# Optimization experiments

Measured on AMD Instinct MI355X. Metric: run time of the kernel, lower is better.

The kernel has to match this reference:

```python
import jax, jax.numpy as jnp
import numpy as np

B, D = 131072, 256            # batch, n_features
ND, NA = 64, 64               # decision_dim, attention_dim
UN = ND + NA                  # GLU units (feature transformer width)
NSTEPS = 3
RELAX = 1.3                   # relaxation_factor
BN_EPS = 1e-3                 # keras BatchNormalization default epsilon
OUT_DIM = 64
SQRT_HALF = float(np.sqrt(0.5))

def _bn(x, g, b, m, v):
    # inference-mode batch norm with moving statistics
    return (x - m) * jax.lax.rsqrt(v + BN_EPS) * g + b

def _glu(x, W, g, b, m, v):
    h = _bn(x @ W, g, b, m, v)            # [B, 2*UN]
    return h[:, :UN] * jax.nn.sigmoid(h[:, UN:])

def _sparsemax(z):
    zs = -jnp.sort(-z, axis=-1)           # descending sort
    k = jnp.arange(1, z.shape[-1] + 1, dtype=z.dtype)
    zc = jnp.cumsum(zs, axis=-1)
    kz = jnp.sum((1.0 + k * zs > zc).astype(jnp.int32), axis=-1, keepdims=True)
    tau = (jnp.take_along_axis(zc, kz - 1, axis=-1) - 1.0) / kz.astype(z.dtype)
    return jnp.maximum(z - tau, 0.0)

def _shared_block(x, W0, W1, g, b, m, v):
    # input dim D != UN -> omit first residual
    h = _glu(x, W0, g[0], b[0], m[0], v[0])
    h2 = _glu(h, W1, g[1], b[1], m[1], v[1])
    return SQRT_HALF * (h + h2)

def _dep_block(x, W, g, b, m, v):
    # input dim UN == UN -> residual on every layer
    for i in range(2):
        h = _glu(x, W[i], g[i], b[i], m[i], v[i])
        x = SQRT_HALF * (x + h)
    return x

def setup_inputs() -> dict:
    key = jax.random.key(0)
    ks = jax.random.split(key, 16)
    s_in = 1.0 / np.sqrt(D)
    s_un = 1.0 / np.sqrt(UN)
    s_na = 1.0 / np.sqrt(NA)
    def bn_params(k, shape):
        k1, k2 = jax.random.split(k)
        return (jax.random.uniform(k1, shape, jnp.float32, 0.5, 1.5),
                0.1 * jax.random.normal(k2, shape, jnp.float32),
                jnp.zeros(shape, jnp.float32), jnp.ones(shape, jnp.float32))
    in_g, in_b, in_m, in_v = bn_params(ks[0], (D,))
    sh_W0 = s_in * jax.random.normal(ks[1], (D, 2 * UN), jnp.float32)
    sh_W1 = s_un * jax.random.normal(ks[2], (UN, 2 * UN), jnp.float32)
    sh_g, sh_b, sh_m, sh_v = bn_params(ks[3], (2, 2 * UN))
    dep_W = s_un * jax.random.normal(ks[4], (NSTEPS + 1, 2, UN, 2 * UN), jnp.float32)
    dep_g, dep_b, dep_m, dep_v = bn_params(ks[5], (NSTEPS + 1, 2, 2 * UN))
    at_W = s_na * jax.random.normal(ks[6], (NSTEPS, NA, D), jnp.float32)
    at_g, at_b, at_m, at_v = bn_params(ks[7], (NSTEPS, D))
    Wout = (1.0 / np.sqrt(ND)) * jax.random.normal(ks[8], (ND, OUT_DIM), jnp.float32)
    inputs = jax.random.normal(ks[9], (B, D), jnp.float32)
    return dict(inputs=inputs, in_g=in_g, in_b=in_b, in_m=in_m, in_v=in_v,
                sh_W0=sh_W0, sh_W1=sh_W1, sh_g=sh_g, sh_b=sh_b, sh_m=sh_m, sh_v=sh_v,
                dep_W=dep_W, dep_g=dep_g, dep_b=dep_b, dep_m=dep_m, dep_v=dep_v,
                at_W=at_W, at_g=at_g, at_b=at_b, at_m=at_m, at_v=at_v, Wout=Wout)

def reference(inputs, in_g, in_b, in_m, in_v, sh_W0, sh_W1, sh_g, sh_b, sh_m, sh_v,
              dep_W, dep_g, dep_b, dep_m, dep_v, at_W, at_g, at_b, at_m, at_v, Wout):
    features = _bn(inputs, in_g, in_b, in_m, in_v)          # initial BN, [B, D]
    # initial feature transformer (step 0 split, only attention part used)
    x = _shared_block(features, sh_W0, sh_W1, sh_g, sh_b, sh_m, sh_v)
    x = _dep_block(x, dep_W[0], dep_g[0], dep_b[0], dep_m[0], dep_v[0])
    a = x[:, ND:]                                           # [B, NA]
    prior = jnp.ones_like(features)
    out_agg = jnp.zeros((inputs.shape[0], ND), inputs.dtype)
    for s in range(NSTEPS):
        logits = _bn(a @ at_W[s], at_g[s], at_b[s], at_m[s], at_v[s])  # [B, D]
        mask = _sparsemax(prior * logits)
        prior = prior * (RELAX - mask)
        x = _shared_block(mask * features, sh_W0, sh_W1, sh_g, sh_b, sh_m, sh_v)
        x = _dep_block(x, dep_W[s + 1], dep_g[s + 1], dep_b[s + 1], dep_m[s + 1], dep_v[s + 1])
        out_agg = out_agg + jax.nn.relu(x[:, :ND])
        a = x[:, ND:]
    return out_agg @ Wout                                   # [B, OUT_DIM]
```

## Files before the change

kernel.cpp:

```cpp
#include <hip/hip_runtime.h>
#include <hip/hip_bf16.h>
#include <hip/hip_fp16.h>

typedef unsigned short u16;
typedef __attribute__((ext_vector_type(8))) short short8;
typedef __attribute__((ext_vector_type(4))) float f32x4;

#define BN_EPS    1e-3f
#define RELAX     1.3f
#define SQRT_HALF 0.7071067811865476f

#define PK_G0_US     0
#define PK_G1_US     65536
#define PK_DEP_US    98304
#define PK_AT_US     360448
#define PK_WOUT_US   409600
#define PK_WOUTLO_US 413696
#define OFF_SHIFT 835584
#define OFF_SCALE 848896
#define OFF_INSC  862208
#define OFF_INSH  863232

__device__ __forceinline__ u16 f2bf(float x){
  unsigned u = __float_as_uint(x);
  return (u16)((u + 0x7fffu + ((u >> 16) & 1u)) >> 16);
}
__device__ __forceinline__ float bf2f(u16 h){ return __uint_as_float(((unsigned)h) << 16); }
__device__ __forceinline__ float sigm(float x){ return 1.0f / (1.0f + __expf(-x)); }
__device__ __forceinline__ f32x4 splat4(float x){ f32x4 v; v[0]=x; v[1]=x; v[2]=x; v[3]=x; return v; }

__device__ __forceinline__ unsigned pk2(float a, float b){
  float2 t; t.x = a; t.y = b;
  union { __hip_bfloat162 h; unsigned u; } v;
  v.h = __float22bfloat162_rn(t);
  return v.u;
}
__device__ __forceinline__ f32x4 unpk4(uint2 p){
  f32x4 r;
  r[0] = __uint_as_float(p.x << 16);
  r[1] = __uint_as_float(p.x & 0xffff0000u);
  r[2] = __uint_as_float(p.y << 16);
  r[3] = __uint_as_float(p.y & 0xffff0000u);
  return r;
}
__device__ __forceinline__ float2 h2f2(unsigned u){
  union { unsigned u; __half2 h; } v; v.u = u;
  return __half22float2(v.h);
}
__device__ __forceinline__ unsigned f22h2(float a, float b){
  union { __half2 h; unsigned u; } v; v.h = __floats2half2_rn(a, b);
  return v.u;
}

__global__ void prep_bn(
  const float* in_g, const float* in_b, const float* in_m, const float* in_v,
  const float* sh_g, const float* sh_b, const float* sh_m, const float* sh_v,
  const float* dep_g, const float* dep_b, const float* dep_m, const float* dep_v,
  const float* at_g, const float* at_b, const float* at_m, const float* at_v,
  float* shiftT, float* scaleT, float* inSc, float* inSh)
{
  int r = blockIdx.x, f = threadIdx.x;
  if (r < 13) {
    const float *g, *bb, *mm, *vv;
    if (r < 2)       { g = sh_g + r*256;        bb = sh_b + r*256;        mm = sh_m + r*256;        vv = sh_v + r*256; }
    else if (r < 10) { int j = r-2;  g = dep_g + j*256; bb = dep_b + j*256; mm = dep_m + j*256; vv = dep_v + j*256; }
    else             { int j = r-10; g = at_g  + j*256; bb = at_b  + j*256; mm = at_m  + j*256; vv = at_v  + j*256; }
    float sc = g[f] * rsqrtf(vv[f] + BN_EPS);
    scaleT[r*256 + f] = sc;
    shiftT[r*256 + f] = bb[f] - mm[f]*sc;
  } else {
    float sc = in_g[f] * rsqrtf(in_v[f] + BN_EPS);
    inSc[f] = sc;
    inSh[f] = in_b[f] - in_m[f]*sc;
  }
}

__global__ void prep_pack(
  const float* sh_W0, const float* sh_W1, const float* dep_W,
  const float* at_W, const float* Wout, const float* scaleT, u16* pk)
{
  int c = blockIdx.x*256 + threadIdx.x;
  const float* W; int K, Nout, srow, base; bool lo = false;
  if (c < 8192)       { W = sh_W0; K = 256; Nout = 256; srow = 0;  base = 0; }
  else if (c < 12288) { W = sh_W1; K = 128; Nout = 256; srow = 1;  base = 8192; }
  else if (c < 45056) { int j = (c-12288) >> 12; W = dep_W + j*32768; K = 128; Nout = 256; srow = 2+j;  base = 12288 + j*4096; }
  else if (c < 51200) { int j = (c-45056) >> 11; W = at_W  + j*16384; K = 64;  Nout = 256; srow = 10+j; base = 45056 + j*2048; }
  else if (c < 51712) { W = Wout; K = 64; Nout = 64; srow = -1; base = 51200; }
  else                { W = Wout; K = 64; Nout = 64; srow = -1; base = 51712; lo = true; }
  int local = c - base;
  int lane  = local & 63;
  int t     = local >> 6;
  int KS    = K >> 5;
  int lsh   = (K == 256) ? 3 : (K == 128) ? 2 : 1;
  int ks    = t & (KS - 1);
  int mf    = t >> lsh;
  int feat  = mf*16 + (lane & 15);
  int k0    = ks*32 + ((lane >> 4) << 3);
  float scl = (srow < 0) ? 1.0f : scaleT[srow*256 + feat];
  u16 v[8];
  #pragma unroll
  for (int j = 0; j < 8; ++j) {
    float x = W[(size_t)(k0 + j)*Nout + feat] * scl;
    u16 h = f2bf(x);
    if (lo) h = f2bf(x - bf2f(h));
    v[j] = h;
  }
  ushort4* d4 = (ushort4*)(pk + (size_t)c*8);
  ushort4 p0; p0.x=v[0]; p0.y=v[1]; p0.z=v[2]; p0.w=v[3];
  ushort4 p1; p1.x=v[4]; p1.y=v[5]; p1.z=v[6]; p1.w=v[7];
  d4[0] = p0; d4[1] = p1;
}

template<int KS, int LDB, int KOFF>
__device__ __forceinline__ void gemm4(const u16* __restrict__ pk, const u16* bufB,
                                      int w, int l15, int lg, int swzv, f32x4 acc[4][2])
{
  const int lane = lg*16 + l15;
  short8 ae[4], be[2], ao[4], bo[2];
  #pragma unroll
  for (int nf = 0; nf < 2; ++nf) {
    int idx = (nf*16 + l15)*LDB + KOFF + lg*8;
    be[nf] = *(const short8*)(bufB + (idx ^ swzv));
  }
  #pragma unroll
  for (int mi = 0; mi < 4; ++mi)
    ae[mi] = *(const short8*)(pk + (size_t)(((w + 4*mi)*KS)*64 + lane)*8);

  #pragma unroll 1
  for (int ks = 0; ks < KS; ks += 2) {
    #pragma unroll
    for (int nf = 0; nf < 2; ++nf) {
      int idx = (nf*16 + l15)*LDB + KOFF + (ks+1)*32 + lg*8;
      bo[nf] = *(const short8*)(bufB + (idx ^ swzv));
    }
    #pragma unroll
    for (int mi = 0; mi < 4; ++mi)
      ao[mi] = *(const short8*)(pk + (size_t)(((w + 4*mi)*KS + ks + 1)*64 + lane)*8);
    #pragma unroll
    for (int mi = 0; mi < 4; ++mi) {
      acc[mi][0] = __builtin_amdgcn_mfma_f32_16x16x32_bf16(ae[mi], be[0], acc[mi][0], 0, 0, 0);
      acc[mi][1] = __builtin_amdgcn_mfma_f32_16x16x32_bf16(ae[mi], be[1], acc[mi][1], 0, 0, 0);
    }
    if (ks + 2 < KS) {
      #pragma unroll
      for (int nf = 0; nf < 2; ++nf) {
        int idx = (nf*16 + l15)*LDB + KOFF + (ks+2)*32 + lg*8;
        be[nf] = *(const short8*)(bufB + (idx ^ swzv));
      }
      #pragma unroll
      for (int mi = 0; mi < 4; ++mi)
        ae[mi] = *(const short8*)(pk + (size_t)(((w + 4*mi)*KS + ks + 2)*64 + lane)*8);
    }
    #pragma unroll
    for (int mi = 0; mi < 4; ++mi) {
      acc[mi][0] = __builtin_amdgcn_mfma_f32_16x16x32_bf16(ao[mi], bo[0], acc[mi][0], 0, 0, 0);
      acc[mi][1] = __builtin_amdgcn_mfma_f32_16x16x32_bf16(ao[mi], bo[1], acc[mi][1], 0, 0, 0);
    }
  }
}

__device__ __forceinline__ void zero4(f32x4 acc[4][2]){
  #pragma unroll
  for (int mi = 0; mi < 4; ++mi)
    #pragma unroll
    for (int nf = 0; nf < 2; ++nf)
      acc[mi][nf] = splat4(0.0f);
}

__device__ __forceinline__ void glu_epi4(const f32x4 acc[4][2], const float* __restrict__ shrow,
                                         int w, int lg, f32x4 h[2][2])
{
  #pragma unroll
  for (int mi = 0; mi < 2; ++mi) {
    const int f0 = (w + 4*mi)*16 + lg*4;
    const f32x4 bh = *(const f32x4*)(shrow + f0);
    const f32x4 bg = *(const f32x4*)(shrow + f0 + 128);
    #pragma unroll
    for (int nf = 0; nf < 2; ++nf)
      #pragma unroll
      for (int c = 0; c < 4; ++c) {
        float v = acc[mi][nf][c] + bh[c];
        float g = acc[mi+2][nf][c] + bg[c];
        h[mi][nf][c] = v * sigm(g);
      }
  }
}

__device__ __forceinline__ void write_half(u16* dst, const f32x4 v[2][2], int w, int l15, int lg, int swzv)
{
  #pragma unroll
  for (int mi = 0; mi < 2; ++mi) {
    const int f0 = (w + 4*mi)*16 + lg*4;
    #pragma unroll
    for (int nf = 0; nf < 2; ++nf) {
      const int s = nf*16 + l15;
      uint2 p;
      p.x = pk2(v[mi][nf][0], v[mi][nf][1]);
      p.y = pk2(v[mi][nf][2], v[mi][nf][3]);
      *(uint2*)(dst + ((s*128 + f0) ^ swzv)) = p;
    }
  }
}

__device__ __forceinline__ void shared_dep(const u16* __restrict__ pk, const float* __restrict__ shiftT,
                                           const u16* binput, u16* big, u16* hbuf, int inv,
                                           int w, int l15, int lg, int swzv)
{
  f32x4 acc[4][2];
  zero4(acc);
  gemm4<8, 256, 0>(pk + PK_G0_US, binput, w, l15, lg, swzv, acc);
  {
    f32x4 h[2][2];
    glu_epi4(acc, shiftT + 0, w, lg, h);
    write_half(hbuf, h, w, l15, lg, swzv);
  }
  __syncthreads();

  zero4(acc);
  gemm4<4, 128, 0>(pk + PK_G1_US, hbuf, w, l15, lg, swzv, acc);
  {
    f32x4 h2[2][2];
    glu_epi4(acc, shiftT + 256, w, lg, h2);
    f32x4 xv[2][2];
    #pragma unroll
    for (int mi = 0; mi < 2; ++mi) {
      const int f0 = (w + 4*mi)*16 + lg*4;
      #pragma unroll
      for (int nf = 0; nf < 2; ++nf) {
        const int s = nf*16 + l15;
        uint2 hp = *(const uint2*)(hbuf + ((s*128 + f0) ^ swzv));
        f32x4 hv = unpk4(hp);
        xv[mi][nf] = (hv + h2[mi][nf]) * SQRT_HALF;
      }
    }
    write_half(big, xv, w, l15, lg, swzv);
  }
  __syncthreads();

  const u16* xin = big;
  u16* xout = big + 4096;
  #pragma unroll
  for (int i = 0; i < 2; ++i) {
    zero4(acc);
    gemm4<4, 128, 0>(pk + PK_DEP_US + (inv*2 + i)*32768, xin, w, l15, lg, swzv, acc);
    f32x4 hd[2][2];
    glu_epi4(acc, shiftT + (2 + inv*2 + i)*256, w, lg, hd);
    #pragma unroll
    for (int mi = 0; mi < 2; ++mi) {
      const int f0 = (w + 4*mi)*16 + lg*4;
      #pragma unroll
      for (int nf = 0; nf < 2; ++nf) {
        const int s = nf*16 + l15;
        uint2 xp = *(const uint2*)(xin + ((s*128 + f0) ^ swzv));
        f32x4 xo = unpk4(xp);
        hd[mi][nf] = (xo + hd[mi][nf]) * SQRT_HALF;
      }
    }
    write_half(xout, hd, w, l15, lg, swzv);
    __syncthreads();
    const u16* t = xin; xin = xout; xout = (u16*)t;
  }
}

__global__ void __launch_bounds__(256, 2)
tabnet_main(const float* __restrict__ inp, const u16* __restrict__ pk,
            const float* __restrict__ shiftT, const float* __restrict__ inSc,
            const float* __restrict__ inSh, float* __restrict__ out)
{
  __shared__ __align__(16) u16 feat[32*256];
  __shared__ __align__(16) u16 big[32*256];
  __shared__ __align__(16) u16 hbuf[32*128];
  __shared__ unsigned priorS[16*256];
  __shared__ float    aggS[8*256];
  float2* red2 = (float2*)hbuf;

  const int tid  = threadIdx.x;
  const int w    = tid >> 6;
  const int lane = tid & 63;
  const int l15  = lane & 15, lg = lane >> 4;
  const int swzv = (l15 & 7) << 3;
  const long long row0 = (long long)blockIdx.x * 32;

  {
    const int f = lane*4;
    const f32x4 sc = *(const f32x4*)(inSc + f);
    const f32x4 sh = *(const f32x4*)(inSh + f);
    #pragma unroll
    for (int j = 0; j < 8; ++j) {
      const int s = j*4 + w;
      f32x4 v = *(const f32x4*)(inp + (row0 + s)*256 + f);
      uint2 p;
      p.x = pk2(v[0]*sc[0] + sh[0], v[1]*sc[1] + sh[1]);
      p.y = pk2(v[2]*sc[2] + sh[2], v[3]*sc[3] + sh[3]);
      *(uint2*)(feat + ((s*256 + f) ^ ((s & 7) << 3))) = p;
    }
  }
  {
    const unsigned one2 = 0x3c003c00u;
    #pragma unroll
    for (int j = 0; j < 16; ++j) priorS[j*256 + tid] = one2;
    #pragma unroll
    for (int j = 0; j < 8; ++j) aggS[j*256 + tid] = 0.0f;
  }
  __syncthreads();

  shared_dep(pk, shiftT, feat, big, hbuf, 0, w, l15, lg, swzv);

  #pragma unroll 1
  for (int st = 0; st < 3; ++st) {
    f32x4 z[4][2];
    zero4(z);
    gemm4<2, 128, 64>(pk + PK_AT_US + st*16384, big, w, l15, lg, swzv, z);
    #pragma unroll
    for (int mi = 0; mi < 4; ++mi) {
      const f32x4 bz = *(const f32x4*)(shiftT + (10 + st)*256 + (w + 4*mi)*16 + lg*4);
      #pragma unroll
      for (int nf = 0; nf < 2; ++nf) {
        float2 p0 = h2f2(priorS[((mi<<2)|(nf<<1)|0)*256 + tid]);
        float2 p1 = h2f2(priorS[((mi<<2)|(nf<<1)|1)*256 + tid]);
        z[mi][nf][0] = (z[mi][nf][0] + bz[0]) * p0.x;
        z[mi][nf][1] = (z[mi][nf][1] + bz[1]) * p0.y;
        z[mi][nf][2] = (z[mi][nf][2] + bz[2]) * p1.x;
        z[mi][nf][3] = (z[mi][nf][3] + bz[3]) * p1.y;
      }
    }

    float tau[2];
    {
      #pragma unroll
      for (int nf = 0; nf < 2; ++nf) {
        float m = -1e30f;
        #pragma unroll
        for (int mi = 0; mi < 4; ++mi)
          #pragma unroll
          for (int c = 0; c < 4; ++c) m = fmaxf(m, z[mi][nf][c]);
        m = fmaxf(m, __shfl_xor(m, 16, 64));
        m = fmaxf(m, __shfl_xor(m, 32, 64));
        if (lg == 0) { int si = nf*16 + l15; red2[si*9 + w].x = m; }
      }
      __syncthreads();
      #pragma unroll
      for (int nf = 0; nf < 2; ++nf) {
        const int si = nf*16 + l15;
        float m = fmaxf(fmaxf(red2[si*9+0].x, red2[si*9+1].x),
                        fmaxf(red2[si*9+2].x, red2[si*9+3].x));
        tau[nf] = m - 1.0f;
      }
    }

    int buf = 0;
    #pragma unroll 1
    for (int it = 0; it < 12; ++it) {
      buf ^= 1;
      float S[2], C[2];
      #pragma unroll
      for (int nf = 0; nf < 2; ++nf) {
        f32x4 s4 = splat4(0.0f), c4 = splat4(0.0f);
        #pragma unroll
        for (int mi = 0; mi < 4; ++mi)
          #pragma unroll
          for (int c = 0; c < 4; ++c) {
            float d = z[mi][nf][c] - tau[nf];
            s4[c] += fmaxf(d, 0.0f);
            c4[c] += (d > 0.0f) ? 1.0f : 0.0f;
          }
        float S_ = (s4[0] + s4[1]) + (s4[2] + s4[3]);
        float C_ = (c4[0] + c4[1]) + (c4[2] + c4[3]);
        S_ += __shfl_xor(S_, 16, 64); S_ += __shfl_xor(S_, 32, 64);
        C_ += __shfl_xor(C_, 16, 64); C_ += __shfl_xor(C_, 32, 64);
        S[nf] = S_; C[nf] = C_;
      }
      if (lg == 0) {
        #pragma unroll
        for (int nf = 0; nf < 2; ++nf) {
          int si = nf*16 + l15;
          float2 p; p.x = S[nf]; p.y = C[nf];
          red2[buf*288 + si*9 + w] = p;
        }
      }
      __syncthreads();
      bool ok = true;
      float tauN[2];
      #pragma unroll
      for (int nf = 0; nf < 2; ++nf) {
        const int si = nf*16 + l15;
        float Ss = 0.0f, Cs = 0.0f;
        #pragma unroll
        for (int i = 0; i < 4; ++i) { float2 p = red2[buf*288 + si*9 + i]; Ss += p.x; Cs += p.y; }
        ok = ok && (fabsf(Ss - 1.0f) < 1e-5f);
        tauN[nf] = tau[nf] + (Ss - 1.0f) / Cs;
      }
      if (__all(ok)) break;
      #pragma unroll
      for (int nf = 0; nf < 2; ++nf) tau[nf] = tauN[nf];
    }

    #pragma unroll
    for (int mi = 0; mi < 4; ++mi) {
      const int f0 = (w + 4*mi)*16 + lg*4;
      #pragma unroll
      for (int nf = 0; nf < 2; ++nf) {
        const int si = nf*16 + l15;
        ushort4 fv = *(const ushort4*)(feat + ((si*256 + f0) ^ swzv));
        float m0 = fmaxf(z[mi][nf][0] - tau[nf], 0.0f);
        float m1 = fmaxf(z[mi][nf][1] - tau[nf], 0.0f);
        float m2 = fmaxf(z[mi][nf][2] - tau[nf], 0.0f);
        float m3 = fmaxf(z[mi][nf][3] - tau[nf], 0.0f);
        const int j0 = ((mi<<2)|(nf<<1)|0)*256 + tid;
        const int j1 = ((mi<<2)|(nf<<1)|1)*256 + tid;
        float2 p0 = h2f2(priorS[j0]);
        float2 p1 = h2f2(priorS[j1]);
        priorS[j0] = f22h2(p0.x * (RELAX - m0), p0.y * (RELAX - m1));
        priorS[j1] = f22h2(p1.x * (RELAX - m2), p1.y * (RELAX - m3));
        uint2 p;
        p.x = pk2(bf2f(fv.x) * m0, bf2f(fv.y) * m1);
        p.y = pk2(bf2f(fv.z) * m2, bf2f(fv.w) * m3);
        *(uint2*)(big + ((si*256 + f0) ^ swzv)) = p;
      }
    }
    __syncthreads();

    shared_dep(pk, shiftT, big, big, hbuf, st + 1, w, l15, lg, swzv);

    #pragma unroll
    for (int nf = 0; nf < 2; ++nf) {
      const int si = nf*16 + l15;
      const int f0 = w*16 + lg*4;
      uint2 xp = *(const uint2*)(big + ((si*128 + f0) ^ swzv));
      f32x4 xv = unpk4(xp);
      #pragma unroll
      for (int c = 0; c < 4; ++c)
        aggS[(nf*4 + c)*256 + tid] += fmaxf(xv[c], 0.0f);
    }
  }

  __syncthreads();
  {
    #pragma unroll
    for (int nf = 0; nf < 2; ++nf) {
      const int si = nf*16 + l15;
      const int f0 = w*16 + lg*4;
      float a0 = aggS[(nf*4+0)*256 + tid];
      float a1 = aggS[(nf*4+1)*256 + tid];
      float a2 = aggS[(nf*4+2)*256 + tid];
      float a3 = aggS[(nf*4+3)*256 + tid];
      ushort4 hi, lo;
      u16 h0 = f2bf(a0); hi.x = h0; lo.x = f2bf(a0 - bf2f(h0));
      u16 h1 = f2bf(a1); hi.y = h1; lo.y = f2bf(a1 - bf2f(h1));
      u16 h2v = f2bf(a2); hi.z = h2v; lo.z = f2bf(a2 - bf2f(h2v));
      u16 h3 = f2bf(a3); hi.w = h3; lo.w = f2bf(a3 - bf2f(h3));
      *(ushort4*)(big + ((si*64 + f0) ^ swzv)) = hi;
      *(ushort4*)(big + 2048 + ((si*64 + f0) ^ swzv)) = lo;
    }
  }
  __syncthreads();

  {
    const int lane64 = lg*16 + l15;
    f32x4 facc[2];
    facc[0] = splat4(0.0f); facc[1] = splat4(0.0f);
    #pragma unroll
    for (int ks = 0; ks < 2; ++ks) {
      short8 aHi = *(const short8*)(pk + PK_WOUT_US   + (size_t)((w*2 + ks)*64 + lane64)*8);
      short8 aLo = *(const short8*)(pk + PK_WOUTLO_US + (size_t)((w*2 + ks)*64 + lane64)*8);
      #pragma unroll
      for (int j = 0; j < 2; ++j) {
        const int si = j*16 + l15;
        short8 bHi = *(const short8*)(big + ((si*64 + ks*32 + lg*8) ^ swzv));
        short8 bLo = *(const short8*)(big + 2048 + ((si*64 + ks*32 + lg*8) ^ swzv));
        facc[j] = __builtin_amdgcn_mfma_f32_16x16x32_bf16(aHi, bHi, facc[j], 0, 0, 0);
        facc[j] = __builtin_amdgcn_mfma_f32_16x16x32_bf16(aHi, bLo, facc[j], 0, 0, 0);
        facc[j] = __builtin_amdgcn_mfma_f32_16x16x32_bf16(aLo, bHi, facc[j], 0, 0, 0);
      }
    }
    #pragma unroll
    for (int j = 0; j < 2; ++j) {
      const int si = j*16 + l15;
      *(f32x4*)(out + (row0 + si)*64 + w*16 + lg*4) = facc[j];
    }
  }
}

extern "C" void kernel_launch(void* const* d_in, const int* in_sizes, int n_in,
                              void* d_out, int out_size, void* d_ws, size_t ws_size,
                              hipStream_t stream)
{
  const float* inp   = (const float*)d_in[0];
  const float* in_g  = (const float*)d_in[1];
  const float* in_b  = (const float*)d_in[2];
  const float* in_m  = (const float*)d_in[3];
  const float* in_v  = (const float*)d_in[4];
  const float* sh_W0 = (const float*)d_in[5];
  const float* sh_W1 = (const float*)d_in[6];
  const float* sh_g  = (const float*)d_in[7];
  const float* sh_b  = (const float*)d_in[8];
  const float* sh_m  = (const float*)d_in[9];
  const float* sh_v  = (const float*)d_in[10];
  const float* dep_W = (const float*)d_in[11];
  const float* dep_g = (const float*)d_in[12];
  const float* dep_b = (const float*)d_in[13];
  const float* dep_m = (const float*)d_in[14];
  const float* dep_v = (const float*)d_in[15];
  const float* at_W  = (const float*)d_in[16];
  const float* at_g  = (const float*)d_in[17];
  const float* at_b  = (const float*)d_in[18];
  const float* at_m  = (const float*)d_in[19];
  const float* at_v  = (const float*)d_in[20];
  const float* Wout  = (const float*)d_in[21];

  unsigned char* ws = (unsigned char*)d_ws;
  u16*   pk     = (u16*)ws;
  float* shiftT = (float*)(ws + OFF_SHIFT);
  float* scaleT = (float*)(ws + OFF_SCALE);
  float* inSc   = (float*)(ws + OFF_INSC);
  float* inSh   = (float*)(ws + OFF_INSH);

  hipLaunchKernelGGL(prep_bn, dim3(14), dim3(256), 0, stream,
                     in_g, in_b, in_m, in_v, sh_g, sh_b, sh_m, sh_v,
                     dep_g, dep_b, dep_m, dep_v, at_g, at_b, at_m, at_v,
                     shiftT, scaleT, inSc, inSh);
  hipLaunchKernelGGL(prep_pack, dim3(204), dim3(256), 0, stream,
                     sh_W0, sh_W1, dep_W, at_W, Wout, scaleT, pk);
  hipLaunchKernelGGL(tabnet_main, dim3(4096), dim3(256), 0, stream,
                     inp, pk, shiftT, inSc, inSh, (float*)d_out);
}
```

Measured before the change: 533.2 us.

## Transpose sparsemax logits through LDS so each row is reduced within one wave

The attention logits are staged through shared memory (aliased with the big/hbuf buffers) and re-read so that each group of 8 lanes owns a whole row, and the prior is stored in a matching row-major layout. The sparsemax threshold iterations then reduce with intra-wave shuffles only, which removes the per-iteration __syncthreads and cross-wave reduction buffer. The cost is an extra LDS write and read of the logits plus two additional barriers per step, and a larger-footprint shared-memory union.

```diff
diff --git a/kernel.cpp b/kernel.cpp
--- a/kernel.cpp
+++ b/kernel.cpp
@@ -268,17 +268,21 @@
             const float* __restrict__ inSh, float* __restrict__ out)
 {
   __shared__ __align__(16) u16 feat[32*256];
-  __shared__ __align__(16) u16 big[32*256];
-  __shared__ __align__(16) u16 hbuf[32*128];
-  __shared__ unsigned priorS[16*256];
+  __shared__ __align__(16) u16 uni[16640];
+  __shared__ unsigned priorT[32*132];
   __shared__ float    aggS[8*256];
-  float2* red2 = (float2*)hbuf;
+  u16*   big  = uni;
+  u16*   hbuf = uni + 8192;
+  float* zbuf = (float*)uni;
 
   const int tid  = threadIdx.x;
   const int w    = tid >> 6;
   const int lane = tid & 63;
   const int l15  = lane & 15, lg = lane >> 4;
   const int swzv = (l15 & 7) << 3;
+  const int a    = lane >> 3;
+  const int b    = lane & 7;
+  const int s_own = w*8 + a;
   const long long row0 = (long long)blockIdx.x * 32;
 
   {
@@ -296,9 +300,12 @@
     }
   }
   {
-    const unsigned one2 = 0x3c003c00u;
-    #pragma unroll
-    for (int j = 0; j < 16; ++j) priorS[j*256 + tid] = one2;
+    #pragma unroll
+    for (int j = 0; j < 8; ++j) {
+      const int c = (b ^ a) + 8*j;
+      uint2 one; one.x = 0x3c003c00u; one.y = 0x3c003c00u;
+      *(uint2*)(priorT + s_own*132 + 2*c) = one;
+    }
     #pragma unroll
     for (int j = 0; j < 8; ++j) aggS[j*256 + tid] = 0.0f;
   }
@@ -311,112 +318,84 @@
     f32x4 z[4][2];
     zero4(z);
     gemm4<2, 128, 64>(pk + PK_AT_US + st*16384, big, w, l15, lg, swzv, z);
+    __syncthreads();
+
     #pragma unroll
     for (int mi = 0; mi < 4; ++mi) {
-      const f32x4 bz = *(const f32x4*)(shiftT + (10 + st)*256 + (w + 4*mi)*16 + lg*4);
+      const int F0 = (w + 4*mi)*16 + lg*4;
       #pragma unroll
       for (int nf = 0; nf < 2; ++nf) {
-        float2 p0 = h2f2(priorS[((mi<<2)|(nf<<1)|0)*256 + tid]);
-        float2 p1 = h2f2(priorS[((mi<<2)|(nf<<1)|1)*256 + tid]);
-        z[mi][nf][0] = (z[mi][nf][0] + bz[0]) * p0.x;
-        z[mi][nf][1] = (z[mi][nf][1] + bz[1]) * p0.y;
-        z[mi][nf][2] = (z[mi][nf][2] + bz[2]) * p1.x;
-        z[mi][nf][3] = (z[mi][nf][3] + bz[3]) * p1.y;
-      }
-    }
-
-    float tau[2];
+        const int s = nf*16 + l15;
+        *(f32x4*)(zbuf + s*260 + F0) = z[mi][nf];
+      }
+    }
+    __syncthreads();
+
+    f32x4 zT[8];
+    float tau;
     {
-      #pragma unroll
-      for (int nf = 0; nf < 2; ++nf) {
-        float m = -1e30f;
-        #pragma unroll
-        for (int mi = 0; mi < 4; ++mi)
-          #pragma unroll
-          for (int c = 0; c < 4; ++c) m = fmaxf(m, z[mi][nf][c]);
-        m = fmaxf(m, __shfl_xor(m, 16, 64));
-        m = fmaxf(m, __shfl_xor(m, 32, 64));
-        if (lg == 0) { int si = nf*16 + l15; red2[si*9 + w].x = m; }
-      }
-      __syncthreads();
-      #pragma unroll
-      for (int nf = 0; nf < 2; ++nf) {
-        const int si = nf*16 + l15;
-        float m = fmaxf(fmaxf(red2[si*9+0].x, red2[si*9+1].x),
-                        fmaxf(red2[si*9+2].x, red2[si*9+3].x));
-        tau[nf] = m - 1.0f;
-      }
-    }
-
-    int buf = 0;
+      const float* bias = shiftT + (10 + st)*256;
+      float mx = -1e30f;
+      #pragma unroll
+      for (int j = 0; j < 8; ++j) {
+        const int c = (b ^ a) + 8*j;
+        const int f = 4*c;
+        f32x4 zv = *(const f32x4*)(zbuf + s_own*260 + f);
+        const f32x4 bz = *(const f32x4*)(bias + f);
+        uint2 pr = *(const uint2*)(priorT + s_own*132 + 2*c);
+        float2 p0 = h2f2(pr.x), p1 = h2f2(pr.y);
+        zv[0] = (zv[0] + bz[0]) * p0.x;
+        zv[1] = (zv[1] + bz[1]) * p0.y;
+        zv[2] = (zv[2] + bz[2]) * p1.x;
+        zv[3] = (zv[3] + bz[3]) * p1.y;
+        zT[j] = zv;
+        mx = fmaxf(mx, fmaxf(fmaxf(zv[0], zv[1]), fmaxf(zv[2], zv[3])));
+      }
+      mx = fmaxf(mx, __shfl_xor(mx, 1, 64));
+      mx = fmaxf(mx, __shfl_xor(mx, 2, 64));
+      mx = fmaxf(mx, __shfl_xor(mx, 4, 64));
+      tau = mx - 1.0f;
+    }
+
     #pragma unroll 1
     for (int it = 0; it < 12; ++it) {
-      buf ^= 1;
-      float S[2], C[2];
-      #pragma unroll
-      for (int nf = 0; nf < 2; ++nf) {
-        f32x4 s4 = splat4(0.0f), c4 = splat4(0.0f);
+      float S = 0.0f, C = 0.0f;
+      #pragma unroll
+      for (int j = 0; j < 8; ++j)
         #pragma unroll
-        for (int mi = 0; mi < 4; ++mi)
-          #pragma unroll
-          for (int c = 0; c < 4; ++c) {
-            float d = z[mi][nf][c] - tau[nf];
-            s4[c] += fmaxf(d, 0.0f);
-            c4[c] += (d > 0.0f) ? 1.0f : 0.0f;
-          }
-        float S_ = (s4[0] + s4[1]) + (s4[2] + s4[3]);
-        float C_ = (c4[0] + c4[1]) + (c4[2] + c4[3]);
-        S_ += __shfl_xor(S_, 16, 64); S_ += __shfl_xor(S_, 32, 64);
-        C_ += __shfl_xor(C_, 16, 64); C_ += __shfl_xor(C_, 32, 64);
-        S[nf] = S_; C[nf] = C_;
-      }
-      if (lg == 0) {
-        #pragma unroll
-        for (int nf = 0; nf < 2; ++nf) {
-          int si = nf*16 + l15;
-          float2 p; p.x = S[nf]; p.y = C[nf];
-          red2[buf*288 + si*9 + w] = p;
+        for (int c4 = 0; c4 < 4; ++c4) {
+          float d = zT[j][c4] - tau;
+          S += fmaxf(d, 0.0f);
+          C += (d > 0.0f) ? 1.0f : 0.0f;
         }
-      }
-      __syncthreads();
-      bool ok = true;
-      float tauN[2];
-      #pragma unroll
-      for (int nf = 0; nf < 2; ++nf) {
-        const int si = nf*16 + l15;
-        float Ss = 0.0f, Cs = 0.0f;
-        #pragma unroll
-        for (int i = 0; i < 4; ++i) { float2 p = red2[buf*288 + si*9 + i]; Ss += p.x; Cs += p.y; }
-        ok = ok && (fabsf(Ss - 1.0f) < 1e-5f);
-        tauN[nf] = tau[nf] + (Ss - 1.0f) / Cs;
-      }
-      if (__all(ok)) break;
-      #pragma unroll
-      for (int nf = 0; nf < 2; ++nf) tau[nf] = tauN[nf];
-    }
-
-    #pragma unroll
-    for (int mi = 0; mi < 4; ++mi) {
-      const int f0 = (w + 4*mi)*16 + lg*4;
-      #pragma unroll
-      for (int nf = 0; nf < 2; ++nf) {
-        const int si = nf*16 + l15;
-        ushort4 fv = *(const ushort4*)(feat + ((si*256 + f0) ^ swzv));
-        float m0 = fmaxf(z[mi][nf][0] - tau[nf], 0.0f);
-        float m1 = fmaxf(z[mi][nf][1] - tau[nf], 0.0f);
-        float m2 = fmaxf(z[mi][nf][2] - tau[nf], 0.0f);
-        float m3 = fmaxf(z[mi][nf][3] - tau[nf], 0.0f);
-        const int j0 = ((mi<<2)|(nf<<1)|0)*256 + tid;
-        const int j1 = ((mi<<2)|(nf<<1)|1)*256 + tid;
-        float2 p0 = h2f2(priorS[j0]);
-        float2 p1 = h2f2(priorS[j1]);
-        priorS[j0] = f22h2(p0.x * (RELAX - m0), p0.y * (RELAX - m1));
-        priorS[j1] = f22h2(p1.x * (RELAX - m2), p1.y * (RELAX - m3));
-        uint2 p;
-        p.x = pk2(bf2f(fv.x) * m0, bf2f(fv.y) * m1);
-        p.y = pk2(bf2f(fv.z) * m2, bf2f(fv.w) * m3);
-        *(uint2*)(big + ((si*256 + f0) ^ swzv)) = p;
-      }
+      S += __shfl_xor(S, 1, 64); C += __shfl_xor(C, 1, 64);
+      S += __shfl_xor(S, 2, 64); C += __shfl_xor(C, 2, 64);
+      S += __shfl_xor(S, 4, 64); C += __shfl_xor(C, 4, 64);
+      if (__all(fabsf(S - 1.0f) < 1e-5f)) break;
+      tau += (S - 1.0f) / C;
+    }
+
+    __syncthreads();
+
+    #pragma unroll
+    for (int j = 0; j < 8; ++j) {
+      const int c = (b ^ a) + 8*j;
+      const int f = 4*c;
+      float m0 = fmaxf(zT[j][0] - tau, 0.0f);
+      float m1 = fmaxf(zT[j][1] - tau, 0.0f);
+      float m2 = fmaxf(zT[j][2] - tau, 0.0f);
+      float m3 = fmaxf(zT[j][3] - tau, 0.0f);
+      uint2 pr = *(const uint2*)(priorT + s_own*132 + 2*c);
+      float2 p0 = h2f2(pr.x), p1 = h2f2(pr.y);
+      pr.x = f22h2(p0.x*(RELAX - m0), p0.y*(RELAX - m1));
+      pr.y = f22h2(p1.x*(RELAX - m2), p1.y*(RELAX - m3));
+      *(uint2*)(priorT + s_own*132 + 2*c) = pr;
+      const int idx = (s_own*256 + f) ^ (a << 3);
+      ushort4 fv = *(const ushort4*)(feat + idx);
+      uint2 o;
+      o.x = pk2(bf2f(fv.x)*m0, bf2f(fv.y)*m1);
+      o.y = pk2(bf2f(fv.z)*m2, bf2f(fv.w)*m3);
+      *(uint2*)(big + idx) = o;
     }
     __syncthreads();
 
```

Result: faster. 508.3 us (-4.7%).
